# Kernel optimization log

Measured on AMD Instinct MI355X. Metric: run time of the kernel, lower is better.

## Reference

```python
import jax, jax.numpy as jnp
import numpy as np

SIGMA_BOOST = 2.0   # sparse-hyper util.SIGMA_BOOST
EPSILON = 1e-6      # sparse-hyper util.EPSILON (10e-7)
B, N = 512, 16384   # batch, size


def setup_inputs() -> dict:
    key = jax.random.key(0)
    k1, k2, k3, k4, k5 = jax.random.split(key, 5)
    return {
        "x": jax.random.normal(k1, (B, N), jnp.float32),
        "noise": jax.random.normal(k2, (B, N, 2), jnp.float32),
        "pmeans": jax.random.normal(k3, (N, 2), jnp.float32),
        "psigmas": jax.random.normal(k4, (N,), jnp.float32),
        "pvalues": jax.random.normal(k5, (N,), jnp.float32),
    }


def reference(x, noise, pmeans, psigmas, pvalues):
    b, n = x.shape
    s = jnp.float32(n)  # square size (n, n); both dims equal
    # hyper(): transform_means = sigmoid * (size-1); transform_sigmas = (softplus(.+boost)+eps) * size
    means = jax.nn.sigmoid(pmeans)[None] * (s - 1.0)                    # (1, n, 2) -> bcast (b, n, 2)
    sigmas = (jax.nn.softplus(psigmas + SIGMA_BOOST) + EPSILON)[None, :, None] * s  # (1, n, 1)
    # Normal(means, sigmas).sample() -- non-differentiable sample
    samples = jax.lax.stop_gradient(means + sigmas * noise)             # (b, n, 2)
    # round, clamp to [0, n-1]
    indices = jnp.clip(jnp.round(samples).astype(jnp.int32), 0, n - 1)  # (b, n, 2)
    rows, cols = indices[..., 0], indices[..., 1]                       # (b, n) each
    values = jnp.broadcast_to(pvalues[None, :], (b, n))
    # sparse.contract: y[b, rows[b,t]] += values[b,t] * x[b, cols[b,t]]
    contrib = values * jnp.take_along_axis(x, cols, axis=1)             # (b, n)
    y = jnp.zeros((b, n), x.dtype).at[jnp.arange(b)[:, None], rows].add(contrib)
    return y
```

## Files before the change

### kernel.cpp

```cpp
#include <hip/hip_runtime.h>
#include <math.h>

#define SIGMA_BOOST 2.0f
#define EPSILON 1e-6f

typedef float vfloat4 __attribute__((ext_vector_type(4)));

__global__ void params_kernel(const float2* __restrict__ pmeans,
                              const float* __restrict__ psigmas,
                              const float* __restrict__ pvalues,
                              float4* __restrict__ params, int N) {
    int t = blockIdx.x * blockDim.x + threadIdx.x;
    if (t >= N) return;
    float2 pm = pmeans[t];
    float scale = (float)(N - 1);
    float m0 = __fmul_rn(__fdiv_rn(1.0f, __fadd_rn(1.0f, expf(-pm.x))), scale);
    float m1 = __fmul_rn(__fdiv_rn(1.0f, __fadd_rn(1.0f, expf(-pm.y))), scale);
    float z  = __fadd_rn(psigmas[t], SIGMA_BOOST);
    float sp = __fadd_rn(fmaxf(z, 0.0f), log1pf(expf(-fabsf(z))));
    float sg = __fmul_rn(__fadd_rn(sp, EPSILON), (float)N);
    params[t] = make_float4(m0, m1, sg, pvalues[t]);
}

template <bool INLINE_PARAMS>
__launch_bounds__(1024, 8)
__global__ void contract_kernel(const float* __restrict__ x,
                                const float2* __restrict__ noise,
                                const float4* __restrict__ params,
                                const float2* __restrict__ pmeans,
                                const float* __restrict__ psigmas,
                                const float* __restrict__ pvalues,
                                float* __restrict__ y, int N) {
    extern __shared__ float ly[];
    const int b = blockIdx.x;
    const int tid = threadIdx.x;
    const int nthr = blockDim.x;

    float4* ly4 = (float4*)ly;
    const int n4 = N >> 2;
    for (int i = tid; i < n4; i += nthr) ly4[i] = make_float4(0.f, 0.f, 0.f, 0.f);
    __syncthreads();

    const float* xb = x + (size_t)b * N;
    const float fN1 = (float)(N - 1);

    if (!INLINE_PARAMS && (N % (4 * nthr)) == 0) {
        const vfloat4* nb4 = (const vfloat4*)(noise + (size_t)b * N);
        const int npairs = N >> 1;
        for (int base = 0; base < npairs; base += 2 * nthr) {
            const int p0 = base + tid;
            const int p1 = base + nthr + tid;
            vfloat4 nz0 = __builtin_nontemporal_load(&nb4[p0]);
            vfloat4 nz1 = __builtin_nontemporal_load(&nb4[p1]);
            float4 pa = params[2 * p0];
            float4 pb = params[2 * p0 + 1];
            float4 pc = params[2 * p1];
            float4 pd = params[2 * p1 + 1];

            float sA0 = __fadd_rn(pa.x, __fmul_rn(pa.z, nz0.x));
            float sA1 = __fadd_rn(pa.y, __fmul_rn(pa.z, nz0.y));
            float sB0 = __fadd_rn(pb.x, __fmul_rn(pb.z, nz0.z));
            float sB1 = __fadd_rn(pb.y, __fmul_rn(pb.z, nz0.w));
            float sC0 = __fadd_rn(pc.x, __fmul_rn(pc.z, nz1.x));
            float sC1 = __fadd_rn(pc.y, __fmul_rn(pc.z, nz1.y));
            float sD0 = __fadd_rn(pd.x, __fmul_rn(pd.z, nz1.z));
            float sD1 = __fadd_rn(pd.y, __fmul_rn(pd.z, nz1.w));

            int rA = (int)fminf(fmaxf(rintf(sA0), 0.0f), fN1);
            int cA = (int)fminf(fmaxf(rintf(sA1), 0.0f), fN1);
            int rB = (int)fminf(fmaxf(rintf(sB0), 0.0f), fN1);
            int cB = (int)fminf(fmaxf(rintf(sB1), 0.0f), fN1);
            int rC = (int)fminf(fmaxf(rintf(sC0), 0.0f), fN1);
            int cC = (int)fminf(fmaxf(rintf(sC1), 0.0f), fN1);
            int rD = (int)fminf(fmaxf(rintf(sD0), 0.0f), fN1);
            int cD = (int)fminf(fmaxf(rintf(sD1), 0.0f), fN1);

            float xA = xb[cA];
            float xB = xb[cB];
            float xC = xb[cC];
            float xD = xb[cD];

            atomicAdd(&ly[rA], __fmul_rn(pa.w, xA));
            atomicAdd(&ly[rB], __fmul_rn(pb.w, xB));
            atomicAdd(&ly[rC], __fmul_rn(pc.w, xC));
            atomicAdd(&ly[rD], __fmul_rn(pd.w, xD));
        }
    } else {
        const float2* nb = noise + (size_t)b * N;
        for (int t = tid; t < N; t += nthr) {
            float m0, m1, sg, pv;
            if (INLINE_PARAMS) {
                float2 pm = pmeans[t];
                float scale = (float)(N - 1);
                m0 = __fmul_rn(__fdiv_rn(1.0f, __fadd_rn(1.0f, expf(-pm.x))), scale);
                m1 = __fmul_rn(__fdiv_rn(1.0f, __fadd_rn(1.0f, expf(-pm.y))), scale);
                float z  = __fadd_rn(psigmas[t], SIGMA_BOOST);
                float sp = __fadd_rn(fmaxf(z, 0.0f), log1pf(expf(-fabsf(z))));
                sg = __fmul_rn(__fadd_rn(sp, EPSILON), (float)N);
                pv = pvalues[t];
            } else {
                float4 p = params[t];
                m0 = p.x; m1 = p.y; sg = p.z; pv = p.w;
            }
            float2 nz = nb[t];
            float s0 = __fadd_rn(m0, __fmul_rn(sg, nz.x));
            float s1 = __fadd_rn(m1, __fmul_rn(sg, nz.y));
            int row = (int)fminf(fmaxf(rintf(s0), 0.0f), fN1);
            int col = (int)fminf(fmaxf(rintf(s1), 0.0f), fN1);
            float contrib = __fmul_rn(pv, xb[col]);
            atomicAdd(&ly[row], contrib);
        }
    }
    __syncthreads();

    const vfloat4* lv4 = (const vfloat4*)ly;
    vfloat4* yb4 = (vfloat4*)(y + (size_t)b * N);
    for (int i = tid; i < n4; i += nthr)
        __builtin_nontemporal_store(lv4[i], &yb4[i]);
}

extern "C" void kernel_launch(void* const* d_in, const int* in_sizes, int n_in,
                              void* d_out, int out_size, void* d_ws, size_t ws_size,
                              hipStream_t stream) {
    const float*  x       = (const float*)d_in[0];
    const float2* noise   = (const float2*)d_in[1];
    const float2* pmeans  = (const float2*)d_in[2];
    const float*  psigmas = (const float*)d_in[3];
    const float*  pvalues = (const float*)d_in[4];
    float* y = (float*)d_out;

    const int N = in_sizes[3];
    const int B = in_sizes[0] / N;

    const size_t params_bytes = (size_t)N * sizeof(float4);
    const bool use_ws = (ws_size >= params_bytes) && (d_ws != nullptr);

    const int block = 1024;
    const size_t lds_bytes = (size_t)N * sizeof(float);

    if (use_ws) {
        float4* params = (float4*)d_ws;
        params_kernel<<<(N + 255) / 256, 256, 0, stream>>>(pmeans, psigmas,
                                                           pvalues, params, N);
        contract_kernel<false><<<B, block, lds_bytes, stream>>>(
            x, noise, params, nullptr, nullptr, nullptr, y, N);
    } else {
        contract_kernel<true><<<B, block, lds_bytes, stream>>>(
            x, noise, nullptr, pmeans, psigmas, pvalues, y, N);
    }
}
```

Measured before the change: 161.8 us.

## Stage x row into LDS and gather from shared memory in new kernel

Adds a contract kernel that loads each batch row of x into LDS next to the accumulator, so the random column gathers read shared memory instead of global or L2. It also unrolls to four noise pairs per thread per iteration to keep more loads in flight. The LDS footprint doubles to 128KB per block, which lowers occupancy to one block per CU. That cuts latency hiding for the streaming noise loads.

```diff
diff --git a/kernel.cpp b/kernel.cpp
--- a/kernel.cpp
+++ b/kernel.cpp
@@ -22,6 +22,111 @@
     params[t] = make_float4(m0, m1, sg, pvalues[t]);
 }
 
+__launch_bounds__(1024, 4)
+__global__ void contract_staged(const float* __restrict__ x,
+                                const float2* __restrict__ noise,
+                                const float4* __restrict__ params,
+                                float* __restrict__ y, int N) {
+    extern __shared__ float lds[];
+    float* ly = lds;
+    float* lx = lds + N;
+    const int b = blockIdx.x;
+    const int tid = threadIdx.x;
+    const int nthr = blockDim.x;
+    const int n4 = N >> 2;
+
+    float4* ly4 = (float4*)ly;
+    vfloat4* lx4 = (vfloat4*)lx;
+    const vfloat4* xb4 = (const vfloat4*)(x + (size_t)b * N);
+    for (int i = tid; i < n4; i += nthr) {
+        ly4[i] = make_float4(0.f, 0.f, 0.f, 0.f);
+        lx4[i] = xb4[i];
+    }
+    __syncthreads();
+
+    const float fN1 = (float)(N - 1);
+    const vfloat4* nb4 = (const vfloat4*)(noise + (size_t)b * N);
+    const int npairs = N >> 1;
+
+    for (int base = 0; base < npairs; base += 4 * nthr) {
+        const int p0 = base + tid;
+        const int p1 = p0 + nthr;
+        const int p2 = p1 + nthr;
+        const int p3 = p2 + nthr;
+
+        vfloat4 nz0 = __builtin_nontemporal_load(&nb4[p0]);
+        vfloat4 nz1 = __builtin_nontemporal_load(&nb4[p1]);
+        vfloat4 nz2 = __builtin_nontemporal_load(&nb4[p2]);
+        vfloat4 nz3 = __builtin_nontemporal_load(&nb4[p3]);
+        float4 pa = params[2 * p0];
+        float4 pb = params[2 * p0 + 1];
+        float4 pc = params[2 * p1];
+        float4 pd = params[2 * p1 + 1];
+        float4 pe = params[2 * p2];
+        float4 pf = params[2 * p2 + 1];
+        float4 pg = params[2 * p3];
+        float4 ph = params[2 * p3 + 1];
+
+        float sA0 = __fadd_rn(pa.x, __fmul_rn(pa.z, nz0.x));
+        float sA1 = __fadd_rn(pa.y, __fmul_rn(pa.z, nz0.y));
+        float sB0 = __fadd_rn(pb.x, __fmul_rn(pb.z, nz0.z));
+        float sB1 = __fadd_rn(pb.y, __fmul_rn(pb.z, nz0.w));
+        float sC0 = __fadd_rn(pc.x, __fmul_rn(pc.z, nz1.x));
+        float sC1 = __fadd_rn(pc.y, __fmul_rn(pc.z, nz1.y));
+        float sD0 = __fadd_rn(pd.x, __fmul_rn(pd.z, nz1.z));
+        float sD1 = __fadd_rn(pd.y, __fmul_rn(pd.z, nz1.w));
+        float sE0 = __fadd_rn(pe.x, __fmul_rn(pe.z, nz2.x));
+        float sE1 = __fadd_rn(pe.y, __fmul_rn(pe.z, nz2.y));
+        float sF0 = __fadd_rn(pf.x, __fmul_rn(pf.z, nz2.z));
+        float sF1 = __fadd_rn(pf.y, __fmul_rn(pf.z, nz2.w));
+        float sG0 = __fadd_rn(pg.x, __fmul_rn(pg.z, nz3.x));
+        float sG1 = __fadd_rn(pg.y, __fmul_rn(pg.z, nz3.y));
+        float sH0 = __fadd_rn(ph.x, __fmul_rn(ph.z, nz3.z));
+        float sH1 = __fadd_rn(ph.y, __fmul_rn(ph.z, nz3.w));
+
+        int rA = (int)fminf(fmaxf(rintf(sA0), 0.0f), fN1);
+        int cA = (int)fminf(fmaxf(rintf(sA1), 0.0f), fN1);
+        int rB = (int)fminf(fmaxf(rintf(sB0), 0.0f), fN1);
+        int cB = (int)fminf(fmaxf(rintf(sB1), 0.0f), fN1);
+        int rC = (int)fminf(fmaxf(rintf(sC0), 0.0f), fN1);
+        int cC = (int)fminf(fmaxf(rintf(sC1), 0.0f), fN1);
+        int rD = (int)fminf(fmaxf(rintf(sD0), 0.0f), fN1);
+        int cD = (int)fminf(fmaxf(rintf(sD1), 0.0f), fN1);
+        int rE = (int)fminf(fmaxf(rintf(sE0), 0.0f), fN1);
+        int cE = (int)fminf(fmaxf(rintf(sE1), 0.0f), fN1);
+        int rF = (int)fminf(fmaxf(rintf(sF0), 0.0f), fN1);
+        int cF = (int)fminf(fmaxf(rintf(sF1), 0.0f), fN1);
+        int rG = (int)fminf(fmaxf(rintf(sG0), 0.0f), fN1);
+        int cG = (int)fminf(fmaxf(rintf(sG1), 0.0f), fN1);
+        int rH = (int)fminf(fmaxf(rintf(sH0), 0.0f), fN1);
+        int cH = (int)fminf(fmaxf(rintf(sH1), 0.0f), fN1);
+
+        float xA = lx[cA];
+        float xB = lx[cB];
+        float xC = lx[cC];
+        float xD = lx[cD];
+        float xE = lx[cE];
+        float xF = lx[cF];
+        float xG = lx[cG];
+        float xH = lx[cH];
+
+        atomicAdd(&ly[rA], __fmul_rn(pa.w, xA));
+        atomicAdd(&ly[rB], __fmul_rn(pb.w, xB));
+        atomicAdd(&ly[rC], __fmul_rn(pc.w, xC));
+        atomicAdd(&ly[rD], __fmul_rn(pd.w, xD));
+        atomicAdd(&ly[rE], __fmul_rn(pe.w, xE));
+        atomicAdd(&ly[rF], __fmul_rn(pf.w, xF));
+        atomicAdd(&ly[rG], __fmul_rn(pg.w, xG));
+        atomicAdd(&ly[rH], __fmul_rn(ph.w, xH));
+    }
+    __syncthreads();
+
+    const vfloat4* lv4 = (const vfloat4*)ly;
+    vfloat4* yb4 = (vfloat4*)(y + (size_t)b * N);
+    for (int i = tid; i < n4; i += nthr)
+        __builtin_nontemporal_store(lv4[i], &yb4[i]);
+}
+
 template <bool INLINE_PARAMS>
 __launch_bounds__(1024, 8)
 __global__ void contract_kernel(const float* __restrict__ x,
@@ -44,72 +149,29 @@
     const float* xb = x + (size_t)b * N;
     const float fN1 = (float)(N - 1);
 
-    if (!INLINE_PARAMS && (N % (4 * nthr)) == 0) {
-        const vfloat4* nb4 = (const vfloat4*)(noise + (size_t)b * N);
-        const int npairs = N >> 1;
-        for (int base = 0; base < npairs; base += 2 * nthr) {
-            const int p0 = base + tid;
-            const int p1 = base + nthr + tid;
-            vfloat4 nz0 = __builtin_nontemporal_load(&nb4[p0]);
-            vfloat4 nz1 = __builtin_nontemporal_load(&nb4[p1]);
-            float4 pa = params[2 * p0];
-            float4 pb = params[2 * p0 + 1];
-            float4 pc = params[2 * p1];
-            float4 pd = params[2 * p1 + 1];
-
-            float sA0 = __fadd_rn(pa.x, __fmul_rn(pa.z, nz0.x));
-            float sA1 = __fadd_rn(pa.y, __fmul_rn(pa.z, nz0.y));
-            float sB0 = __fadd_rn(pb.x, __fmul_rn(pb.z, nz0.z));
-            float sB1 = __fadd_rn(pb.y, __fmul_rn(pb.z, nz0.w));
-            float sC0 = __fadd_rn(pc.x, __fmul_rn(pc.z, nz1.x));
-            float sC1 = __fadd_rn(pc.y, __fmul_rn(pc.z, nz1.y));
-            float sD0 = __fadd_rn(pd.x, __fmul_rn(pd.z, nz1.z));
-            float sD1 = __fadd_rn(pd.y, __fmul_rn(pd.z, nz1.w));
-
-            int rA = (int)fminf(fmaxf(rintf(sA0), 0.0f), fN1);
-            int cA = (int)fminf(fmaxf(rintf(sA1), 0.0f), fN1);
-            int rB = (int)fminf(fmaxf(rintf(sB0), 0.0f), fN1);
-            int cB = (int)fminf(fmaxf(rintf(sB1), 0.0f), fN1);
-            int rC = (int)fminf(fmaxf(rintf(sC0), 0.0f), fN1);
-            int cC = (int)fminf(fmaxf(rintf(sC1), 0.0f), fN1);
-            int rD = (int)fminf(fmaxf(rintf(sD0), 0.0f), fN1);
-            int cD = (int)fminf(fmaxf(rintf(sD1), 0.0f), fN1);
-
-            float xA = xb[cA];
-            float xB = xb[cB];
-            float xC = xb[cC];
-            float xD = xb[cD];
-
-            atomicAdd(&ly[rA], __fmul_rn(pa.w, xA));
-            atomicAdd(&ly[rB], __fmul_rn(pb.w, xB));
-            atomicAdd(&ly[rC], __fmul_rn(pc.w, xC));
-            atomicAdd(&ly[rD], __fmul_rn(pd.w, xD));
+    const float2* nb = noise + (size_t)b * N;
+    for (int t = tid; t < N; t += nthr) {
+        float m0, m1, sg, pv;
+        if (INLINE_PARAMS) {
+            float2 pm = pmeans[t];
+            float scale = (float)(N - 1);
+            m0 = __fmul_rn(__fdiv_rn(1.0f, __fadd_rn(1.0f, expf(-pm.x))), scale);
+            m1 = __fmul_rn(__fdiv_rn(1.0f, __fadd_rn(1.0f, expf(-pm.y))), scale);
+            float z  = __fadd_rn(psigmas[t], SIGMA_BOOST);
+            float sp = __fadd_rn(fmaxf(z, 0.0f), log1pf(expf(-fabsf(z))));
+            sg = __fmul_rn(__fadd_rn(sp, EPSILON), (float)N);
+            pv = pvalues[t];
+        } else {
+            float4 p = params[t];
+            m0 = p.x; m1 = p.y; sg = p.z; pv = p.w;
         }
-    } else {
-        const float2* nb = noise + (size_t)b * N;
-        for (int t = tid; t < N; t += nthr) {
-            float m0, m1, sg, pv;
-            if (INLINE_PARAMS) {
-                float2 pm = pmeans[t];
-                float scale = (float)(N - 1);
-                m0 = __fmul_rn(__fdiv_rn(1.0f, __fadd_rn(1.0f, expf(-pm.x))), scale);
-                m1 = __fmul_rn(__fdiv_rn(1.0f, __fadd_rn(1.0f, expf(-pm.y))), scale);
-                float z  = __fadd_rn(psigmas[t], SIGMA_BOOST);
-                float sp = __fadd_rn(fmaxf(z, 0.0f), log1pf(expf(-fabsf(z))));
-                sg = __fmul_rn(__fadd_rn(sp, EPSILON), (float)N);
-                pv = pvalues[t];
-            } else {
-                float4 p = params[t];
-                m0 = p.x; m1 = p.y; sg = p.z; pv = p.w;
-            }
-            float2 nz = nb[t];
-            float s0 = __fadd_rn(m0, __fmul_rn(sg, nz.x));
-            float s1 = __fadd_rn(m1, __fmul_rn(sg, nz.y));
-            int row = (int)fminf(fmaxf(rintf(s0), 0.0f), fN1);
-            int col = (int)fminf(fmaxf(rintf(s1), 0.0f), fN1);
-            float contrib = __fmul_rn(pv, xb[col]);
-            atomicAdd(&ly[row], contrib);
-        }
+        float2 nz = nb[t];
+        float s0 = __fadd_rn(m0, __fmul_rn(sg, nz.x));
+        float s1 = __fadd_rn(m1, __fmul_rn(sg, nz.y));
+        int row = (int)fminf(fmaxf(rintf(s0), 0.0f), fN1);
+        int col = (int)fminf(fmaxf(rintf(s1), 0.0f), fN1);
+        float contrib = __fmul_rn(pv, xb[col]);
+        atomicAdd(&ly[row], contrib);
     }
     __syncthreads();
 
@@ -136,16 +198,31 @@
     const bool use_ws = (ws_size >= params_bytes) && (d_ws != nullptr);
 
     const int block = 1024;
-    const size_t lds_bytes = (size_t)N * sizeof(float);
+    const size_t lds_acc   = (size_t)N * sizeof(float);
+    const size_t lds_stage = 2 * lds_acc;
+
+    bool staged_ok = false;
+    if (use_ws && lds_stage <= 160 * 1024 &&
+        ((N >> 1) % (4 * block)) == 0 && (N % 4) == 0) {
+        hipError_t e = hipFuncSetAttribute(
+            reinterpret_cast<const void*>(contract_staged),
+            hipFuncAttributeMaxDynamicSharedMemorySize, (int)lds_stage);
+        staged_ok = (e == hipSuccess);
+    }
 
     if (use_ws) {
         float4* params = (float4*)d_ws;
         params_kernel<<<(N + 255) / 256, 256, 0, stream>>>(pmeans, psigmas,
                                                            pvalues, params, N);
-        contract_kernel<false><<<B, block, lds_bytes, stream>>>(
-            x, noise, params, nullptr, nullptr, nullptr, y, N);
+        if (staged_ok) {
+            contract_staged<<<B, block, lds_stage, stream>>>(x, noise, params,
+                                                             y, N);
+        } else {
+            contract_kernel<false><<<B, block, lds_acc, stream>>>(
+                x, noise, params, nullptr, nullptr, nullptr, y, N);
+        }
     } else {
-        contract_kernel<true><<<B, block, lds_bytes, stream>>>(
+        contract_kernel<true><<<B, block, lds_acc, stream>>>(
             x, noise, nullptr, pmeans, psigmas, pvalues, y, N);
     }
 }
```

New measurement: 170.8 us. 5.6% more time.
